# Optimization experiments

Hardware: AMD Instinct MI355X
Metric: run time of the kernel (lower is better)

Reference implementation:

```python
import jax, jax.numpy as jnp
import numpy as np

H = 128; L = 4; N_TOTAL = 2500; M = 4; K = 12
S = N_TOTAL * M          # 10000 subgraphs
F = S * K                # 120000 flat nodes
E_INTRA = 2 * F          # 240000 intra-subgraph edges
E_INTER = 16 * N_TOTAL   # 40000 canonical edges
B = 50; VOCAB = 119; MAX_DIST = 32; BN_EPS = 1e-5


def _bn(x, g, b):
    # training-mode BatchNorm1d over rows (biased var, eps=1e-5)
    mu = x.mean(0)
    var = x.var(0)
    return (x - mu) * jax.lax.rsqrt(var + BN_EPS) * g + b


def _gine(x, ei, ea, W1, b1, W2, b2):
    # PyG GINEConv, eps=0: MLP(x + sum_{src->dst} relu(x[src] + e))
    msg = jax.nn.relu(x[ei[0]] + ea)                              # [E,H]
    agg = jax.ops.segment_sum(msg, ei[1], num_segments=x.shape[0])
    h = x + agg
    return jax.nn.relu(h @ W1 + b1) @ W2 + b2


def setup_inputs():
    key = jax.random.key(0)
    ks = list(jax.random.split(key, 32)); it = iter(ks)
    nk = lambda: next(it)
    rn = lambda shape, s=0.05: jax.random.normal(nk(), shape, dtype=jnp.float32) * s
    x_tok = jax.random.randint(nk(), (F,), 0, VOCAB)
    dist = jax.random.randint(nk(), (F,), 0, MAX_DIST + 1)
    node_ids = jax.random.randint(nk(), (F,), 0, N_TOTAL)
    node_ids = jnp.where(jax.random.uniform(nk(), (F,)) < 0.1, -1, node_ids)
    root_flat_idx = jnp.arange(S) * K
    node_ids = node_ids.at[root_flat_idx].set(jnp.arange(S) // M)  # root = canonical node
    valid = node_ids >= 0
    sub_batch = jnp.repeat(jnp.arange(S), K)
    src = jax.random.randint(nk(), (E_INTRA,), 0, F)
    dst = (src // K) * K + jax.random.randint(nk(), (E_INTRA,), 0, K)  # stay inside subgraph
    intra_ei = jnp.stack([src, dst])
    edge_index = jax.random.randint(nk(), (2, E_INTER), 0, N_TOTAL)
    batch_ids = jnp.arange(N_TOTAL) // (N_TOTAL // B)
    lp = -jax.random.uniform(nk(), (S,)) * 3.0                    # log-probs <= 0
    z = lambda *shape: jnp.zeros(shape, jnp.float32)
    o = lambda *shape: jnp.ones(shape, jnp.float32)
    return dict(
        x_tok=x_tok, dist=dist, node_ids=node_ids, valid=valid,
        sub_batch=sub_batch, root_flat_idx=root_flat_idx,
        intra_ei=intra_ei, edge_index=edge_index, batch_ids=batch_ids,
        lp=lp, ea_flat=rn((E_INTRA, H)), edge_attr=rn((E_INTER, H)),
        atom_emb=rn((VOCAB, H)), dist_emb=rn((MAX_DIST + 1, H)),
        logp_w=rn((1, H)), logp_b=z(H),
        intra_W1=rn((L, H, H)), intra_b1=z(L, H),
        intra_W2=rn((L, H, H)), intra_b2=z(L, H),
        intra_bn_g=o(L, H), intra_bn_b=z(L, H),
        self_W=rn((L, H, H)), self_b=z(L, H),
        root_W=rn((L, H, H)), root_b=z(L, H),
        inter_W1=rn((L, H, H)), inter_b1=z(L, H),
        inter_W2=rn((L, H, H)), inter_b2=z(L, H),
        inter_bn_g=o(L, H), inter_bn_b=z(L, H),
        readout_bn_g=o(H), readout_bn_b=z(H),
        alpha_pool=o(1), alpha_inter=o(1),
    )


def reference(x_tok, dist, node_ids, valid, sub_batch, root_flat_idx, intra_ei,
              edge_index, batch_ids, lp, ea_flat, edge_attr, atom_emb, dist_emb,
              logp_w, logp_b, intra_W1, intra_b1, intra_W2, intra_b2,
              intra_bn_g, intra_bn_b, self_W, self_b, root_W, root_b,
              inter_W1, inter_b1, inter_W2, inter_b2, inter_bn_g, inter_bn_b,
              readout_bn_g, readout_bn_b, alpha_pool, alpha_inter):
    valid_f = valid.astype(jnp.float32)[:, None]                  # [F,1]
    is_root_f = jnp.zeros((F, 1), jnp.float32).at[root_flat_idx].set(1.0)
    clamped_ids = jnp.maximum(node_ids, 0)
    # input encoding: atom embedding + BFS-distance PE + log-prob PE
    logp_pe = jax.nn.relu(lp[sub_batch][:, None] * logp_w[0] + logp_b)
    h = (atom_emb[x_tok] + dist_emb[dist] + logp_pe) * valid_f
    # HT inter-root weights, normalized per canonical root id
    root_ids = node_ids[root_flat_idx]                            # [S]
    rv = root_ids >= 0
    rid = jnp.maximum(root_ids, 0)
    w_un = jnp.where(rv, jnp.exp(-alpha_inter[0] * lp), 0.0)
    w_sum = jax.ops.segment_sum(w_un, rid, num_segments=N_TOTAL)
    ht_w = jnp.where(rv, w_un / (w_sum[rid] + 1e-16), 0.0)        # [S]
    for l in range(L):
        h1 = _gine(h, intra_ei, ea_flat, intra_W1[l], intra_b1[l], intra_W2[l], intra_b2[l])
        h1 = _bn(h1, intra_bn_g[l], intra_bn_b[l]) * valid_f
        h_root_bcast = h[sub_batch * K]
        h_non_root = (h @ self_W[l] + self_b[l]) + (h_root_bcast @ root_W[l] + root_b[l])
        # HT-weighted scatter of root reps to canonical nodes
        h_roots = h[root_flat_idx]                                # [S,H]
        h_root_canon = jax.ops.segment_sum(h_roots * ht_w[:, None], rid, num_segments=N_TOTAL)
        h_inter = _gine(h_root_canon, edge_index, edge_attr, inter_W1[l], inter_b1[l], inter_W2[l], inter_b2[l])
        h_inter = _bn(h_inter, inter_bn_g[l], inter_bn_b[l])
        h_inter_bcast = h_inter[clamped_ids] * valid_f
        out = is_root_f * (h1 + h_inter_bcast) + (1.0 - is_root_f) * (h1 + h_non_root)
        h = jax.nn.relu(out) * valid_f                            # dropout p=0
    # HT softmax readout over the m subgraphs of each canonical node
    h_sub = jax.ops.segment_sum(h * valid_f, sub_batch, num_segments=S)
    h_sub_2d = h_sub.reshape(N_TOTAL, M, H)
    w = jax.nn.softmax(-alpha_pool[0] * lp.reshape(N_TOTAL, M), axis=1)
    node_emb = jnp.einsum('nm,nmh->nh', w, h_sub_2d)
    node_emb = _bn(node_emb, readout_bn_g, readout_bn_b)
    return jax.ops.segment_sum(node_emb, batch_ids, num_segments=B)  # [B,H]
```

## Files before the change

### kernel.cpp

```cpp
#include <hip/hip_runtime.h>
#include <math.h>

#define H 128
#define H4 (H/4)
#define KK 12
#define MSUB 4
#define FF 120000
#define SS 10000
#define NN 2500
#define NBATCH 50
#define NLAYER 4
#define EINTRA 240000
#define EINTER 40000
#define HH (H*H)
#define BN_EPS 1e-5f
#define CAP_I 32
#define CAP_E 96

typedef short short8 __attribute__((ext_vector_type(8)));
typedef float floatx4 __attribute__((ext_vector_type(4)));

__device__ __forceinline__ unsigned short f2bf_rne(float x){
  unsigned u = __float_as_uint(x);
  unsigned r = u + 0x7FFFu + ((u >> 16) & 1u);
  return (unsigned short)(r >> 16);
}


__global__ void k_zero(float* __restrict__ p, int n){
  int i = blockIdx.x*256 + threadIdx.x;
  if (i < n) p[i] = 0.f;
}

__global__ void k_zeroi(int* __restrict__ p, int n){
  int i = blockIdx.x*256 + threadIdx.x;
  if (i < n) p[i] = 0;
}


__global__ void k_bucket(const int* __restrict__ dst, int E, int* __restrict__ cnt,
                         int* __restrict__ beid, int cap){
  int e = blockIdx.x*256 + threadIdx.x;
  if (e >= E) return;
  int d = dst[e];
  int p = atomicAdd(&cnt[d], 1);
  if (p < cap) beid[(size_t)d*cap + p] = e;
}


__global__ void k_encode(float* __restrict__ h, const int* __restrict__ xtok,
                         const int* __restrict__ dist, const int* __restrict__ nids,
                         const int* __restrict__ subb, const float* __restrict__ lp,
                         const float* __restrict__ aemb, const float* __restrict__ demb,
                         const float* __restrict__ lw, const float* __restrict__ lb){
  int idx = blockIdx.x*256 + threadIdx.x;
  if (idx >= FF*H4) return;
  int f = idx >> 5; int c = (idx & 31) << 2;
  float vf = (nids[f] >= 0) ? 1.f : 0.f;
  float l = lp[subb[f]];
  float4 a = *(const float4*)(aemb + (size_t)xtok[f]*H + c);
  float4 d = *(const float4*)(demb + (size_t)dist[f]*H + c);
  float4 w = *(const float4*)(lw + c);
  float4 b = *(const float4*)(lb + c);
  float4 o;
  o.x = (a.x + d.x + fmaxf(fmaf(l, w.x, b.x), 0.f)) * vf;
  o.y = (a.y + d.y + fmaxf(fmaf(l, w.y, b.y), 0.f)) * vf;
  o.z = (a.z + d.z + fmaxf(fmaf(l, w.z, b.z), 0.f)) * vf;
  o.w = (a.w + d.w + fmaxf(fmaf(l, w.w, b.w), 0.f)) * vf;
  *(float4*)(h + (size_t)f*H + c) = o;
}


__global__ void k_htw(const int* __restrict__ nids, const int* __restrict__ rfi,
                      const float* __restrict__ lp, const float* __restrict__ alpha,
                      float* __restrict__ htw){
  int n = blockIdx.x*256 + threadIdx.x;
  if (n >= NN) return;
  float a = alpha[0];
  float w[MSUB]; float sum = 0.f;
  #pragma unroll
  for (int m = 0; m < MSUB; ++m){
    int s = n*MSUB + m;
    int rid = nids[rfi[s]];
    float wm = (rid >= 0) ? expf(-a*lp[s]) : 0.f;
    w[m] = wm; sum += wm;
  }
  float inv = 1.f / (sum + 1e-16f);
  #pragma unroll
  for (int m = 0; m < MSUB; ++m) htw[n*MSUB + m] = w[m]*inv;
}


__global__ void k_gine_gather(float* __restrict__ outa, const float* __restrict__ x,
                              const float* __restrict__ ea, const int* __restrict__ cnt,
                              const int* __restrict__ beid, const int* __restrict__ src,
                              int rows, int cap){
  int idx = blockIdx.x*256 + threadIdx.x;
  if (idx >= rows*H4) return;
  int f = idx >> 5; int c = (idx & 31) << 2;
  float4 acc = *(const float4*)(x + (size_t)f*H + c);
  int n = cnt[f]; if (n > cap) n = cap;
  const int* bl = beid + (size_t)f*cap;
  for (int i = 0; i < n; ++i){
    int e = bl[i];
    int s = src[e];
    float4 xv = *(const float4*)(x + (size_t)s*H + c);
    float4 ev = *(const float4*)(ea + (size_t)e*H + c);
    acc.x += fmaxf(xv.x + ev.x, 0.f);
    acc.y += fmaxf(xv.y + ev.y, 0.f);
    acc.z += fmaxf(xv.z + ev.z, 0.f);
    acc.w += fmaxf(xv.w + ev.w, 0.f);
  }
  *(float4*)(outa + (size_t)f*H + c) = acc;
}


__global__ void k_canon(float* __restrict__ canon, const float* __restrict__ h,
                        const float* __restrict__ htw, const int* __restrict__ rfi){
  int idx = blockIdx.x*256 + threadIdx.x;
  if (idx >= NN*H4) return;
  int n = idx >> 5; int c = (idx & 31) << 2;
  float4 acc = make_float4(0.f,0.f,0.f,0.f);
  #pragma unroll
  for (int m = 0; m < MSUB; ++m){
    int s = n*MSUB + m;
    float w = htw[s];
    const float* p = h + (size_t)rfi[s]*H + c;
    acc.x += w*p[0]; acc.y += w*p[1]; acc.z += w*p[2]; acc.w += w*p[3];
  }
  *(float4*)(canon + (size_t)n*H + c) = acc;
}


__global__ __launch_bounds__(256, 2) void k_mm_mfma(
    const float* __restrict__ in, float* __restrict__ out, int rows,
    const float* __restrict__ W, const float* __restrict__ bias,
    int do_relu, const int* __restrict__ gather)
{
  __shared__ __align__(16) short wfrag[2][4][8][64][8];
  int tid = threadIdx.x;
  int w = tid >> 6, l = tid & 63;
  int quad = l >> 4, n15 = l & 15;

  #pragma unroll
  for (int i = 0; i < 8; ++i){
    int c = w + (i << 2);
    int ks = c >> 3, nt = c & 7;
    #pragma unroll
    for (int j = 0; j < 8; ++j){
      int k = ks*32 + quad*8 + j;
      int n = nt*16 + n15;
      float v = W[(size_t)k*H + n];
      unsigned short hb = f2bf_rne(v);
      float hf = __uint_as_float((unsigned)hb << 16);
      unsigned short lb = f2bf_rne(v - hf);
      wfrag[0][ks][nt][l][j] = (short)hb;
      wfrag[1][ks][nt][l][j] = (short)lb;
    }
  }
  __syncthreads();

  int ngroups = (rows + 63) >> 6;
  for (int g = blockIdx.x; g < ngroups; g += gridDim.x){
    int rload = g*64 + w*16 + n15;
    bool okload = rload < rows;
    int ir = okload ? (gather ? gather[rload] : rload) : 0;
    const float* ap = in + (size_t)ir*H + quad*8;

    short8 ah[4], al[4];
    #pragma unroll
    for (int ks = 0; ks < 4; ++ks){
      float4 a0 = okload ? *(const float4*)(ap + ks*32 + 0) : make_float4(0.f,0.f,0.f,0.f);
      float4 a1 = okload ? *(const float4*)(ap + ks*32 + 4) : make_float4(0.f,0.f,0.f,0.f);
      float av[8] = {a0.x,a0.y,a0.z,a0.w,a1.x,a1.y,a1.z,a1.w};
      #pragma unroll
      for (int j = 0; j < 8; ++j){
        unsigned short hb = f2bf_rne(av[j]);
        float hf = __uint_as_float((unsigned)hb << 16);
        ah[ks][j] = (short)hb;
        al[ks][j] = (short)f2bf_rne(av[j] - hf);
      }
    }

    floatx4 acc[8] = {};
    #pragma unroll
    for (int ks = 0; ks < 4; ++ks){
      #pragma unroll
      for (int nt = 0; nt < 8; ++nt){
        short8 bh = *(const short8*)&wfrag[0][ks][nt][l][0];
        short8 bl = *(const short8*)&wfrag[1][ks][nt][l][0];
        acc[nt] = __builtin_amdgcn_mfma_f32_16x16x32_bf16(ah[ks], bh, acc[nt], 0, 0, 0);
        acc[nt] = __builtin_amdgcn_mfma_f32_16x16x32_bf16(al[ks], bh, acc[nt], 0, 0, 0);
        acc[nt] = __builtin_amdgcn_mfma_f32_16x16x32_bf16(ah[ks], bl, acc[nt], 0, 0, 0);
      }
    }

    int rbase = g*64 + w*16 + quad*4;
    #pragma unroll
    for (int nt = 0; nt < 8; ++nt){
      int col = nt*16 + n15;
      float bv = bias[col];
      #pragma unroll
      for (int reg = 0; reg < 4; ++reg){
        int r = rbase + reg;
        if (r < rows){
          float v = acc[nt][reg] + bv;
          if (do_relu) v = fmaxf(v, 0.f);
          out[(size_t)r*H + col] = v;
        }
      }
    }
  }
}


__global__ void k_bnstats(const float* __restrict__ x, int rows, double* __restrict__ stats){
  int g = blockIdx.x*256 + threadIdx.x;
  int c = g & (H-1);
  int rstart = g >> 7;
  int rstride = (gridDim.x*256) >> 7;
  double s = 0.0, s2 = 0.0;
  for (int r = rstart; r < rows; r += rstride){
    float v = x[(size_t)r*H + c];
    s += v; s2 += (double)v*(double)v;
  }
  atomicAdd(&stats[c], s);
  atomicAdd(&stats[H+c], s2);
}

__global__ void k_bnfin(double* __restrict__ stats, int rows, float* __restrict__ muinv){
  int c = threadIdx.x;
  if (c < H){
    double mu = stats[c] / (double)rows;
    double var = stats[H+c] / (double)rows - mu*mu;
    muinv[c]   = (float)mu;
    muinv[H+c] = (float)(1.0 / sqrt(var + (double)BN_EPS));
    stats[c] = 0.0; stats[H+c] = 0.0;
  }
}

__global__ void k_bnapply(float* __restrict__ x, const float* __restrict__ muinv,
                          const float* __restrict__ g, const float* __restrict__ b, int rows){
  int idx = blockIdx.x*256 + threadIdx.x;
  if (idx >= rows*H4) return;
  int r = idx >> 5; int c = (idx & 31) << 2;
  float4 v  = *(const float4*)(x + (size_t)r*H + c);
  float4 mu = *(const float4*)(muinv + c);
  float4 iv = *(const float4*)(muinv + H + c);
  float4 gg = *(const float4*)(g + c);
  float4 bb = *(const float4*)(b + c);
  v.x = (v.x-mu.x)*iv.x*gg.x + bb.x;
  v.y = (v.y-mu.y)*iv.y*gg.y + bb.y;
  v.z = (v.z-mu.z)*iv.z*gg.z + bb.z;
  v.w = (v.w-mu.w)*iv.w*gg.w + bb.w;
  *(float4*)(x + (size_t)r*H + c) = v;
}


__global__ void k_combine(float* __restrict__ h, const float* __restrict__ h1raw,
                          const float* __restrict__ r1, const float* __restrict__ r2,
                          const float* __restrict__ hinter, const float* __restrict__ muinv,
                          const float* __restrict__ bg, const float* __restrict__ bb,
                          const int* __restrict__ nids){
  int idx = blockIdx.x*256 + threadIdx.x;
  if (idx >= FF*H4) return;
  int f = idx >> 5; int c = (idx & 31) << 2;
  int nid = nids[f];
  float vf = (nid >= 0) ? 1.f : 0.f;
  int cid = (nid < 0) ? 0 : nid;
  float4 x  = *(const float4*)(h1raw + (size_t)f*H + c);
  float4 mu = *(const float4*)(muinv + c);
  float4 iv = *(const float4*)(muinv + H + c);
  float4 g4 = *(const float4*)(bg + c);
  float4 b4 = *(const float4*)(bb + c);
  float4 h1;
  h1.x = ((x.x-mu.x)*iv.x*g4.x + b4.x) * vf;
  h1.y = ((x.y-mu.y)*iv.y*g4.y + b4.y) * vf;
  h1.z = ((x.z-mu.z)*iv.z*g4.z + b4.z) * vf;
  h1.w = ((x.w-mu.w)*iv.w*g4.w + b4.w) * vf;
  float4 o;
  if (f % KK == 0){
    float4 hi = *(const float4*)(hinter + (size_t)cid*H + c);
    o.x = h1.x + hi.x*vf; o.y = h1.y + hi.y*vf; o.z = h1.z + hi.z*vf; o.w = h1.w + hi.w*vf;
  } else {
    float4 a  = *(const float4*)(r1 + (size_t)f*H + c);
    float4 rr = *(const float4*)(r2 + (size_t)(f/KK)*H + c);
    o.x = h1.x + a.x + rr.x; o.y = h1.y + a.y + rr.y; o.z = h1.z + a.z + rr.z; o.w = h1.w + a.w + rr.w;
  }
  o.x = fmaxf(o.x,0.f)*vf; o.y = fmaxf(o.y,0.f)*vf; o.z = fmaxf(o.z,0.f)*vf; o.w = fmaxf(o.w,0.f)*vf;
  *(float4*)(h + (size_t)f*H + c) = o;
}


__global__ void k_hsub(float* __restrict__ hsub, const float* __restrict__ h){
  int idx = blockIdx.x*256 + threadIdx.x;
  if (idx >= SS*H4) return;
  int s = idx >> 5; int c = (idx & 31) << 2;
  float4 acc = make_float4(0.f,0.f,0.f,0.f);
  const float* base = h + (size_t)s*KK*H + c;
  #pragma unroll
  for (int k = 0; k < KK; ++k){
    float4 v = *(const float4*)(base + (size_t)k*H);
    acc.x += v.x; acc.y += v.y; acc.z += v.z; acc.w += v.w;
  }
  *(float4*)(hsub + (size_t)s*H + c) = acc;
}

__global__ void k_poolw(float* __restrict__ poolw, const float* __restrict__ lp,
                        const float* __restrict__ alpha){
  int n = blockIdx.x*256 + threadIdx.x;
  if (n >= NN) return;
  float a = alpha[0];
  float s0 = -a*lp[n*MSUB+0], s1 = -a*lp[n*MSUB+1], s2 = -a*lp[n*MSUB+2], s3 = -a*lp[n*MSUB+3];
  float m = fmaxf(fmaxf(s0,s1), fmaxf(s2,s3));
  float e0 = expf(s0-m), e1 = expf(s1-m), e2 = expf(s2-m), e3 = expf(s3-m);
  float sum = e0+e1+e2+e3;
  poolw[n*MSUB+0] = e0/sum; poolw[n*MSUB+1] = e1/sum;
  poolw[n*MSUB+2] = e2/sum; poolw[n*MSUB+3] = e3/sum;
}

__global__ void k_nodeemb(float* __restrict__ nemb, const float* __restrict__ hsub,
                          const float* __restrict__ poolw){
  int idx = blockIdx.x*256 + threadIdx.x;
  if (idx >= NN*H4) return;
  int n = idx >> 5; int c = (idx & 31) << 2;
  float w0 = poolw[n*MSUB+0], w1 = poolw[n*MSUB+1], w2 = poolw[n*MSUB+2], w3 = poolw[n*MSUB+3];
  const float* base = hsub + (size_t)n*MSUB*H + c;
  float4 v0 = *(const float4*)(base + 0*H);
  float4 v1 = *(const float4*)(base + 1*H);
  float4 v2 = *(const float4*)(base + 2*H);
  float4 v3 = *(const float4*)(base + 3*H);
  float4 o;
  o.x = w0*v0.x + w1*v1.x + w2*v2.x + w3*v3.x;
  o.y = w0*v0.y + w1*v1.y + w2*v2.y + w3*v3.y;
  o.z = w0*v0.z + w1*v1.z + w2*v2.z + w3*v3.z;
  o.w = w0*v0.w + w1*v1.w + w2*v2.w + w3*v3.w;
  *(float4*)(nemb + (size_t)n*H + c) = o;
}

__global__ void k_out(float* __restrict__ out, const float* __restrict__ nemb,
                      const float* __restrict__ muinv, const float* __restrict__ g,
                      const float* __restrict__ b){
  int idx = blockIdx.x*256 + threadIdx.x;
  if (idx >= NBATCH*H) return;
  int bi = idx >> 7; int c = idx & (H-1);
  float mu = muinv[c], iv = muinv[H+c], gg = g[c], bb = b[c];
  float acc = 0.f;
  const float* base = nemb + (size_t)bi*(NN/NBATCH)*H + c;
  for (int i = 0; i < NN/NBATCH; ++i)
    acc += (base[(size_t)i*H] - mu)*iv*gg + bb;
  out[idx] = acc;
}


extern "C" void kernel_launch(void* const* d_in, const int* in_sizes, int n_in,
                              void* d_out, int out_size, void* d_ws, size_t ws_size,
                              hipStream_t stream) {
  const int*   x_tok      = (const int*)  d_in[0];
  const int*   dist       = (const int*)  d_in[1];
  const int*   node_ids   = (const int*)  d_in[2];
  const int*   sub_batch  = (const int*)  d_in[4];
  const int*   rfi        = (const int*)  d_in[5];
  const int*   intra_ei   = (const int*)  d_in[6];
  const int*   edge_index = (const int*)  d_in[7];
  const float* lp         = (const float*)d_in[9];
  const float* ea_flat    = (const float*)d_in[10];
  const float* edge_attr  = (const float*)d_in[11];
  const float* atom_emb   = (const float*)d_in[12];
  const float* dist_emb   = (const float*)d_in[13];
  const float* logp_w     = (const float*)d_in[14];
  const float* logp_b     = (const float*)d_in[15];
  const float* intra_W1   = (const float*)d_in[16];
  const float* intra_b1   = (const float*)d_in[17];
  const float* intra_W2   = (const float*)d_in[18];
  const float* intra_b2   = (const float*)d_in[19];
  const float* intra_bn_g = (const float*)d_in[20];
  const float* intra_bn_b = (const float*)d_in[21];
  const float* self_W     = (const float*)d_in[22];
  const float* self_b     = (const float*)d_in[23];
  const float* root_W     = (const float*)d_in[24];
  const float* root_b     = (const float*)d_in[25];
  const float* inter_W1   = (const float*)d_in[26];
  const float* inter_b1   = (const float*)d_in[27];
  const float* inter_W2   = (const float*)d_in[28];
  const float* inter_b2   = (const float*)d_in[29];
  const float* inter_bn_g = (const float*)d_in[30];
  const float* inter_bn_b = (const float*)d_in[31];
  const float* ro_bn_g    = (const float*)d_in[32];
  const float* ro_bn_b    = (const float*)d_in[33];
  const float* alpha_pool = (const float*)d_in[34];
  const float* alpha_inter= (const float*)d_in[35];

  const int* isrc = intra_ei;
  const int* idst = intra_ei + EINTRA;
  const int* esrc = edge_index;
  const int* edst = edge_index + EINTER;

  float* out = (float*)d_out;

  char* ws = (char*)d_ws;
  size_t off = 0;
  auto nxt = [&](size_t bytes) -> void* {
    void* p = ws + off;
    off += (bytes + 255) & ~(size_t)255;
    return p;
  };
  float*  h      = (float*) nxt((size_t)FF*H*4);
  float*  hmid   = (float*) nxt((size_t)FF*H*4);
  float*  tbuf   = (float*) nxt((size_t)FF*H*4);
  float*  r2     = (float*) nxt((size_t)SS*H*4);
  float*  canon  = (float*) nxt((size_t)NN*H*4);
  float*  agg2   = (float*) nxt((size_t)NN*H*4);
  float*  hsub   = (float*) nxt((size_t)SS*H*4);
  float*  nemb   = (float*) nxt((size_t)NN*H*4);
  float*  htw    = (float*) nxt((size_t)SS*4);
  float*  poolw  = (float*) nxt((size_t)NN*MSUB*4);
  double* statsA = (double*)nxt((size_t)2*H*8);
  double* statsB = (double*)nxt((size_t)2*H*8);
  float*  muinvA = (float*) nxt((size_t)2*H*4);
  float*  muinvB = (float*) nxt((size_t)2*H*4);
  int*    icnt   = (int*)   nxt((size_t)FF*4);
  int*    ibeid  = (int*)   nxt((size_t)FF*CAP_I*4);
  int*    ecnt   = (int*)   nxt((size_t)NN*4);
  int*    ebeid  = (int*)   nxt((size_t)NN*CAP_E*4);
  (void)ws_size; (void)n_in; (void)in_sizes; (void)out_size; (void)sub_batch;

  const int G_FH4 = FF*H4/256;
  const int G_SH4 = SS*H4/256;
  const int G_NH4 = (NN*H4 + 255)/256;
  const int G_N   = (NN + 255)/256;
  const int G_MM_F = 512;
  const int G_MM_S = (SS + 63)/64;
  const int G_MM_N = (NN + 63)/64;

  k_zero<<<2, 256, 0, stream>>>((float*)statsA, 2*H*2);
  k_zero<<<2, 256, 0, stream>>>((float*)statsB, 2*H*2);
  k_zeroi<<<(FF+255)/256, 256, 0, stream>>>(icnt, FF);
  k_zeroi<<<G_N, 256, 0, stream>>>(ecnt, NN);

  k_bucket<<<(EINTRA+255)/256, 256, 0, stream>>>(idst, EINTRA, icnt, ibeid, CAP_I);
  k_bucket<<<(EINTER+255)/256, 256, 0, stream>>>(edst, EINTER, ecnt, ebeid, CAP_E);

  k_encode<<<G_FH4, 256, 0, stream>>>(h, x_tok, dist, node_ids, sub_batch, lp,
                                      atom_emb, dist_emb, logp_w, logp_b);
  k_htw<<<G_N, 256, 0, stream>>>(node_ids, rfi, lp, alpha_inter, htw);

  for (int l = 0; l < NLAYER; ++l){
    const float* W1 = intra_W1 + (size_t)l*HH; const float* b1 = intra_b1 + (size_t)l*H;
    const float* W2 = intra_W2 + (size_t)l*HH; const float* b2 = intra_b2 + (size_t)l*H;

    k_gine_gather<<<G_FH4, 256, 0, stream>>>(hmid, h, ea_flat, icnt, ibeid, isrc, FF, CAP_I);
    k_mm_mfma<<<G_MM_F, 256, 0, stream>>>(hmid, tbuf, FF, W1, b1, 1, nullptr);
    k_mm_mfma<<<G_MM_F, 256, 0, stream>>>(tbuf, hmid, FF, W2, b2, 0, nullptr);
    k_bnstats<<<512, 256, 0, stream>>>(hmid, FF, statsA);
    k_bnfin<<<1, 128, 0, stream>>>(statsA, FF, muinvA);

    k_canon<<<G_NH4, 256, 0, stream>>>(canon, h, htw, rfi);
    k_mm_mfma<<<G_MM_S, 256, 0, stream>>>(h, r2, SS, root_W + (size_t)l*HH,
                                          root_b + (size_t)l*H, 0, rfi);

    k_gine_gather<<<G_NH4, 256, 0, stream>>>(agg2, canon, edge_attr, ecnt, ebeid, esrc, NN, CAP_E);
    k_mm_mfma<<<G_MM_N, 256, 0, stream>>>(agg2, tbuf, NN, inter_W1 + (size_t)l*HH,
                                          inter_b1 + (size_t)l*H, 1, nullptr);
    k_mm_mfma<<<G_MM_N, 256, 0, stream>>>(tbuf, agg2, NN, inter_W2 + (size_t)l*HH,
                                          inter_b2 + (size_t)l*H, 0, nullptr);
    k_bnstats<<<128, 256, 0, stream>>>(agg2, NN, statsB);
    k_bnfin<<<1, 128, 0, stream>>>(statsB, NN, muinvB);
    k_bnapply<<<G_NH4, 256, 0, stream>>>(agg2, muinvB, inter_bn_g + (size_t)l*H,
                                         inter_bn_b + (size_t)l*H, NN);

    k_mm_mfma<<<G_MM_F, 256, 0, stream>>>(h, tbuf, FF, self_W + (size_t)l*HH,
                                          self_b + (size_t)l*H, 0, nullptr);
    k_combine<<<G_FH4, 256, 0, stream>>>(h, hmid, tbuf, r2, agg2, muinvA,
                                         intra_bn_g + (size_t)l*H,
                                         intra_bn_b + (size_t)l*H, node_ids);
  }

  k_hsub<<<G_SH4, 256, 0, stream>>>(hsub, h);
  k_poolw<<<G_N, 256, 0, stream>>>(poolw, lp, alpha_pool);
  k_nodeemb<<<G_NH4, 256, 0, stream>>>(nemb, hsub, poolw);
  k_bnstats<<<128, 256, 0, stream>>>(nemb, NN, statsB);
  k_bnfin<<<1, 128, 0, stream>>>(statsB, NN, muinvB);
  k_out<<<(NBATCH*H+255)/256, 256, 0, stream>>>(out, nemb, muinvB, ro_bn_g, ro_bn_b);
}
```

Before: 2.005 ms.

## Fuse combine into self-matmul epilogue, pack edge src ids, prefetch A rows

The separate combine kernel is removed. Its BatchNorm-apply, root/non-root mixing, ReLU and validity masking now run in a new epilogue mode of the MFMA matmul kernel, which writes h in place. This avoids writing and re-reading the full-size self-projection buffer every layer. The edge buckets now store (edge id, src) pairs, which removes a dependent lookup in the gather. The matmul loads its weights with vectorised reads and prefetches the next row group's inputs into registers, at the cost of higher register pressure. The intra bucket capacity drops from 32 to 24, which could truncate edges if any node's in-degree exceeds 24.

```diff
diff --git a/kernel.cpp b/kernel.cpp
--- a/kernel.cpp
+++ b/kernel.cpp
@@ -14,7 +14,7 @@
 #define EINTER 40000
 #define HH (H*H)
 #define BN_EPS 1e-5f
-#define CAP_I 32
+#define CAP_I 24
 #define CAP_E 96
 
 typedef short short8 __attribute__((ext_vector_type(8)));
@@ -38,13 +38,13 @@
 }
 
 
-__global__ void k_bucket(const int* __restrict__ dst, int E, int* __restrict__ cnt,
-                         int* __restrict__ beid, int cap){
+__global__ void k_bucket2(const int* __restrict__ dst, const int* __restrict__ src,
+                          int E, int* __restrict__ cnt, int2* __restrict__ beid, int cap){
   int e = blockIdx.x*256 + threadIdx.x;
   if (e >= E) return;
   int d = dst[e];
   int p = atomicAdd(&cnt[d], 1);
-  if (p < cap) beid[(size_t)d*cap + p] = e;
+  if (p < cap) beid[(size_t)d*cap + p] = make_int2(e, src[e]);
 }
 
 
@@ -93,19 +93,17 @@
 
 __global__ void k_gine_gather(float* __restrict__ outa, const float* __restrict__ x,
                               const float* __restrict__ ea, const int* __restrict__ cnt,
-                              const int* __restrict__ beid, const int* __restrict__ src,
-                              int rows, int cap){
+                              const int2* __restrict__ beid, int rows, int cap){
   int idx = blockIdx.x*256 + threadIdx.x;
   if (idx >= rows*H4) return;
   int f = idx >> 5; int c = (idx & 31) << 2;
   float4 acc = *(const float4*)(x + (size_t)f*H + c);
   int n = cnt[f]; if (n > cap) n = cap;
-  const int* bl = beid + (size_t)f*cap;
+  const int2* bl = beid + (size_t)f*cap;
   for (int i = 0; i < n; ++i){
-    int e = bl[i];
-    int s = src[e];
-    float4 xv = *(const float4*)(x + (size_t)s*H + c);
-    float4 ev = *(const float4*)(ea + (size_t)e*H + c);
+    int2 es = bl[i];
+    float4 xv = *(const float4*)(x + (size_t)es.y*H + c);
+    float4 ev = *(const float4*)(ea + (size_t)es.x*H + c);
     acc.x += fmaxf(xv.x + ev.x, 0.f);
     acc.y += fmaxf(xv.y + ev.y, 0.f);
     acc.z += fmaxf(xv.z + ev.z, 0.f);
@@ -133,9 +131,13 @@
 
 
 __global__ __launch_bounds__(256, 2) void k_mm_mfma(
-    const float* __restrict__ in, float* __restrict__ out, int rows,
+    const float* in, float* out, int rows,
     const float* __restrict__ W, const float* __restrict__ bias,
-    int do_relu, const int* __restrict__ gather)
+    int mode, const int* __restrict__ gather,
+    const float* __restrict__ hmid, const float* __restrict__ r2,
+    const float* __restrict__ hinter, const float* __restrict__ muinv,
+    const float* __restrict__ bg, const float* __restrict__ bb,
+    const int* __restrict__ nids)
 {
   __shared__ __align__(16) short wfrag[2][4][8][64][8];
   int tid = threadIdx.x;
@@ -143,36 +145,49 @@
   int quad = l >> 4, n15 = l & 15;
 
   #pragma unroll
-  for (int i = 0; i < 8; ++i){
-    int c = w + (i << 2);
-    int ks = c >> 3, nt = c & 7;
+  for (int p = 0; p < 16; ++p){
+    int k = p*8 + (tid >> 5);
+    int n = (tid & 31) << 2;
+    float4 v = *(const float4*)(W + (size_t)k*H + n);
+    int ks = k >> 5, qd = (k >> 3) & 3, j = k & 7, nt = n >> 4, l0 = qd*16 + (n & 15);
+    float vv[4] = {v.x, v.y, v.z, v.w};
     #pragma unroll
-    for (int j = 0; j < 8; ++j){
-      int k = ks*32 + quad*8 + j;
-      int n = nt*16 + n15;
-      float v = W[(size_t)k*H + n];
-      unsigned short hb = f2bf_rne(v);
+    for (int q = 0; q < 4; ++q){
+      unsigned short hb = f2bf_rne(vv[q]);
       float hf = __uint_as_float((unsigned)hb << 16);
-      unsigned short lb = f2bf_rne(v - hf);
-      wfrag[0][ks][nt][l][j] = (short)hb;
-      wfrag[1][ks][nt][l][j] = (short)lb;
+      wfrag[0][ks][nt][l0+q][j] = (short)hb;
+      wfrag[1][ks][nt][l0+q][j] = (short)f2bf_rne(vv[q] - hf);
     }
   }
   __syncthreads();
 
   int ngroups = (rows + 63) >> 6;
-  for (int g = blockIdx.x; g < ngroups; g += gridDim.x){
-    int rload = g*64 + w*16 + n15;
-    bool okload = rload < rows;
-    int ir = okload ? (gather ? gather[rload] : rload) : 0;
+
+  float4 cur[8], nxt[8];
+  auto loadA = [&](int gg, float4* buf){
+    int rload = gg*64 + w*16 + n15;
+    bool ok = rload < rows;
+    int ir = ok ? (gather ? gather[rload] : rload) : 0;
     const float* ap = in + (size_t)ir*H + quad*8;
+    #pragma unroll
+    for (int ks = 0; ks < 4; ++ks){
+      buf[2*ks]   = ok ? *(const float4*)(ap + ks*32)     : make_float4(0.f,0.f,0.f,0.f);
+      buf[2*ks+1] = ok ? *(const float4*)(ap + ks*32 + 4) : make_float4(0.f,0.f,0.f,0.f);
+    }
+  };
+
+  int g0 = blockIdx.x;
+  if (g0 < ngroups) loadA(g0, cur);
+
+  for (int g = g0; g < ngroups; g += gridDim.x){
+    int gn = g + gridDim.x;
+    if (gn < ngroups) loadA(gn, nxt);
 
     short8 ah[4], al[4];
     #pragma unroll
     for (int ks = 0; ks < 4; ++ks){
-      float4 a0 = okload ? *(const float4*)(ap + ks*32 + 0) : make_float4(0.f,0.f,0.f,0.f);
-      float4 a1 = okload ? *(const float4*)(ap + ks*32 + 4) : make_float4(0.f,0.f,0.f,0.f);
-      float av[8] = {a0.x,a0.y,a0.z,a0.w,a1.x,a1.y,a1.z,a1.w};
+      float av[8] = {cur[2*ks].x, cur[2*ks].y, cur[2*ks].z, cur[2*ks].w,
+                     cur[2*ks+1].x, cur[2*ks+1].y, cur[2*ks+1].z, cur[2*ks+1].w};
       #pragma unroll
       for (int j = 0; j < 8; ++j){
         unsigned short hb = f2bf_rne(av[j]);
@@ -196,20 +211,56 @@
     }
 
     int rbase = g*64 + w*16 + quad*4;
-    #pragma unroll
-    for (int nt = 0; nt < 8; ++nt){
-      int col = nt*16 + n15;
-      float bv = bias[col];
+    if (mode != 2){
+      #pragma unroll
+      for (int nt = 0; nt < 8; ++nt){
+        int col = nt*16 + n15;
+        float bv = bias[col];
+        #pragma unroll
+        for (int reg = 0; reg < 4; ++reg){
+          int r = rbase + reg;
+          if (r < rows){
+            float v = acc[nt][reg] + bv;
+            if (mode == 1) v = fmaxf(v, 0.f);
+            out[(size_t)r*H + col] = v;
+          }
+        }
+      }
+    } else {
+      int nid4[4], rdiv[4], isroot[4];
       #pragma unroll
       for (int reg = 0; reg < 4; ++reg){
         int r = rbase + reg;
-        if (r < rows){
-          float v = acc[nt][reg] + bv;
-          if (do_relu) v = fmaxf(v, 0.f);
-          out[(size_t)r*H + col] = v;
+        nid4[reg]  = (r < rows) ? nids[r] : -1;
+        rdiv[reg]  = r / KK;
+        isroot[reg] = (r % KK == 0);
+      }
+      #pragma unroll
+      for (int nt = 0; nt < 8; ++nt){
+        int col = nt*16 + n15;
+        float bv = bias[col];
+        float mu = muinv[col], iv = muinv[H+col], gg = bg[col], bbv = bb[col];
+        #pragma unroll
+        for (int reg = 0; reg < 4; ++reg){
+          int r = rbase + reg;
+          if (r < rows){
+            int nid = nid4[reg];
+            float vf = (nid >= 0) ? 1.f : 0.f;
+            int cid = (nid < 0) ? 0 : nid;
+            float xv = hmid[(size_t)r*H + col];
+            float h1 = ((xv - mu)*iv*gg + bbv) * vf;
+            float o;
+            if (isroot[reg]) o = h1 + hinter[(size_t)cid*H + col]*vf;
+            else             o = h1 + (acc[nt][reg] + bv) + r2[(size_t)rdiv[reg]*H + col];
+            o = fmaxf(o, 0.f)*vf;
+            out[(size_t)r*H + col] = o;
+          }
         }
       }
     }
+
+    #pragma unroll
+    for (int i = 0; i < 8; ++i) cur[i] = nxt[i];
   }
 }
 
@@ -254,41 +305,6 @@
   v.z = (v.z-mu.z)*iv.z*gg.z + bb.z;
   v.w = (v.w-mu.w)*iv.w*gg.w + bb.w;
   *(float4*)(x + (size_t)r*H + c) = v;
-}
-
-
-__global__ void k_combine(float* __restrict__ h, const float* __restrict__ h1raw,
-                          const float* __restrict__ r1, const float* __restrict__ r2,
-                          const float* __restrict__ hinter, const float* __restrict__ muinv,
-                          const float* __restrict__ bg, const float* __restrict__ bb,
-                          const int* __restrict__ nids){
-  int idx = blockIdx.x*256 + threadIdx.x;
-  if (idx >= FF*H4) return;
-  int f = idx >> 5; int c = (idx & 31) << 2;
-  int nid = nids[f];
-  float vf = (nid >= 0) ? 1.f : 0.f;
-  int cid = (nid < 0) ? 0 : nid;
-  float4 x  = *(const float4*)(h1raw + (size_t)f*H + c);
-  float4 mu = *(const float4*)(muinv + c);
-  float4 iv = *(const float4*)(muinv + H + c);
-  float4 g4 = *(const float4*)(bg + c);
-  float4 b4 = *(const float4*)(bb + c);
-  float4 h1;
-  h1.x = ((x.x-mu.x)*iv.x*g4.x + b4.x) * vf;
-  h1.y = ((x.y-mu.y)*iv.y*g4.y + b4.y) * vf;
-  h1.z = ((x.z-mu.z)*iv.z*g4.z + b4.z) * vf;
-  h1.w = ((x.w-mu.w)*iv.w*g4.w + b4.w) * vf;
-  float4 o;
-  if (f % KK == 0){
-    float4 hi = *(const float4*)(hinter + (size_t)cid*H + c);
-    o.x = h1.x + hi.x*vf; o.y = h1.y + hi.y*vf; o.z = h1.z + hi.z*vf; o.w = h1.w + hi.w*vf;
-  } else {
-    float4 a  = *(const float4*)(r1 + (size_t)f*H + c);
-    float4 rr = *(const float4*)(r2 + (size_t)(f/KK)*H + c);
-    o.x = h1.x + a.x + rr.x; o.y = h1.y + a.y + rr.y; o.z = h1.z + a.z + rr.z; o.w = h1.w + a.w + rr.w;
-  }
-  o.x = fmaxf(o.x,0.f)*vf; o.y = fmaxf(o.y,0.f)*vf; o.z = fmaxf(o.z,0.f)*vf; o.w = fmaxf(o.w,0.f)*vf;
-  *(float4*)(h + (size_t)f*H + c) = o;
 }
 
 
@@ -420,9 +436,9 @@
   float*  muinvA = (float*) nxt((size_t)2*H*4);
   float*  muinvB = (float*) nxt((size_t)2*H*4);
   int*    icnt   = (int*)   nxt((size_t)FF*4);
-  int*    ibeid  = (int*)   nxt((size_t)FF*CAP_I*4);
+  int2*   ibeid  = (int2*)  nxt((size_t)FF*CAP_I*8);
   int*    ecnt   = (int*)   nxt((size_t)NN*4);
-  int*    ebeid  = (int*)   nxt((size_t)NN*CAP_E*4);
+  int2*   ebeid  = (int2*)  nxt((size_t)NN*CAP_E*8);
   (void)ws_size; (void)n_in; (void)in_sizes; (void)out_size; (void)sub_batch;
 
   const int G_FH4 = FF*H4/256;
@@ -438,8 +454,8 @@
   k_zeroi<<<(FF+255)/256, 256, 0, stream>>>(icnt, FF);
   k_zeroi<<<G_N, 256, 0, stream>>>(ecnt, NN);
 
-  k_bucket<<<(EINTRA+255)/256, 256, 0, stream>>>(idst, EINTRA, icnt, ibeid, CAP_I);
-  k_bucket<<<(EINTER+255)/256, 256, 0, stream>>>(edst, EINTER, ecnt, ebeid, CAP_E);
+  k_bucket2<<<(EINTRA+255)/256, 256, 0, stream>>>(idst, isrc, EINTRA, icnt, ibeid, CAP_I);
+  k_bucket2<<<(EINTER+255)/256, 256, 0, stream>>>(edst, esrc, EINTER, ecnt, ebeid, CAP_E);
 
   k_encode<<<G_FH4, 256, 0, stream>>>(h, x_tok, dist, node_ids, sub_batch, lp,
                                       atom_emb, dist_emb, logp_w, logp_b);
@@ -449,31 +465,36 @@
     const float* W1 = intra_W1 + (size_t)l*HH; const float* b1 = intra_b1 + (size_t)l*H;
     const float* W2 = intra_W2 + (size_t)l*HH; const float* b2 = intra_b2 + (size_t)l*H;
 
-    k_gine_gather<<<G_FH4, 256, 0, stream>>>(hmid, h, ea_flat, icnt, ibeid, isrc, FF, CAP_I);
-    k_mm_mfma<<<G_MM_F, 256, 0, stream>>>(hmid, tbuf, FF, W1, b1, 1, nullptr);
-    k_mm_mfma<<<G_MM_F, 256, 0, stream>>>(tbuf, hmid, FF, W2, b2, 0, nullptr);
+    k_gine_gather<<<G_FH4, 256, 0, stream>>>(hmid, h, ea_flat, icnt, ibeid, FF, CAP_I);
+    k_mm_mfma<<<G_MM_F, 256, 0, stream>>>(hmid, tbuf, FF, W1, b1, 1, nullptr,
+                                          nullptr,nullptr,nullptr,nullptr,nullptr,nullptr,nullptr);
+    k_mm_mfma<<<G_MM_F, 256, 0, stream>>>(tbuf, hmid, FF, W2, b2, 0, nullptr,
+                                          nullptr,nullptr,nullptr,nullptr,nullptr,nullptr,nullptr);
     k_bnstats<<<512, 256, 0, stream>>>(hmid, FF, statsA);
     k_bnfin<<<1, 128, 0, stream>>>(statsA, FF, muinvA);
 
     k_canon<<<G_NH4, 256, 0, stream>>>(canon, h, htw, rfi);
     k_mm_mfma<<<G_MM_S, 256, 0, stream>>>(h, r2, SS, root_W + (size_t)l*HH,
-                                          root_b + (size_t)l*H, 0, rfi);
-
-    k_gine_gather<<<G_NH4, 256, 0, stream>>>(agg2, canon, edge_attr, ecnt, ebeid, esrc, NN, CAP_E);
+                                          root_b + (size_t)l*H, 0, rfi,
+                                          nullptr,nullptr,nullptr,nullptr,nullptr,nullptr,nullptr);
+
+    k_gine_gather<<<G_NH4, 256, 0, stream>>>(agg2, canon, edge_attr, ecnt, ebeid, NN, CAP_E);
     k_mm_mfma<<<G_MM_N, 256, 0, stream>>>(agg2, tbuf, NN, inter_W1 + (size_t)l*HH,
-                                          inter_b1 + (size_t)l*H, 1, nullptr);
+                                          inter_b1 + (size_t)l*H, 1, nullptr,
+                                          nullptr,nullptr,nullptr,nullptr,nullptr,nullptr,nullptr);
     k_mm_mfma<<<G_MM_N, 256, 0, stream>>>(tbuf, agg2, NN, inter_W2 + (size_t)l*HH,
-                                          inter_b2 + (size_t)l*H, 0, nullptr);
+                                          inter_b2 + (size_t)l*H, 0, nullptr,
+                                          nullptr,nullptr,nullptr,nullptr,nullptr,nullptr,nullptr);
     k_bnstats<<<128, 256, 0, stream>>>(agg2, NN, statsB);
     k_bnfin<<<1, 128, 0, stream>>>(statsB, NN, muinvB);
     k_bnapply<<<G_NH4, 256, 0, stream>>>(agg2, muinvB, inter_bn_g + (size_t)l*H,
                                          inter_bn_b + (size_t)l*H, NN);
 
-    k_mm_mfma<<<G_MM_F, 256, 0, stream>>>(h, tbuf, FF, self_W + (size_t)l*HH,
-                                          self_b + (size_t)l*H, 0, nullptr);
-    k_combine<<<G_FH4, 256, 0, stream>>>(h, hmid, tbuf, r2, agg2, muinvA,
-                                         intra_bn_g + (size_t)l*H,
-                                         intra_bn_b + (size_t)l*H, node_ids);
+    k_mm_mfma<<<G_MM_F, 256, 0, stream>>>(h, h, FF, self_W + (size_t)l*HH,
+                                          self_b + (size_t)l*H, 2, nullptr,
+                                          hmid, r2, agg2, muinvA,
+                                          intra_bn_g + (size_t)l*H,
+                                          intra_bn_b + (size_t)l*H, node_ids);
   }
 
   k_hsub<<<G_SH4, 256, 0, stream>>>(hsub, h);
```

Result: slower. 2.637 ms (+31.5%).
